# Performance work log

Hardware: AMD Instinct MI355X
Metric: run time of the kernel (lower is better)

## Reference

```python
import jax, jax.numpy as jnp
import numpy as np

N_NODES = 163842
SEQ_LEN = 9
IN_CH = 32
OUT_CH = 64


def setup_inputs() -> dict:
    key = jax.random.key(0)
    k1, k2, k3 = jax.random.split(key, 3)
    x = jax.random.normal(k1, (N_NODES, IN_CH), dtype=jnp.float32)
    indices = jax.random.randint(k2, (N_NODES, SEQ_LEN), 0, N_NODES, dtype=jnp.int64)
    # xavier_uniform for Linear(IN_CH*SEQ_LEN, OUT_CH)
    fan_in = IN_CH * SEQ_LEN
    limit = float(np.sqrt(6.0 / (fan_in + OUT_CH)))
    W = jax.random.uniform(k3, (OUT_CH, fan_in), dtype=jnp.float32, minval=-limit, maxval=limit)
    b = jnp.zeros((OUT_CH,), dtype=jnp.float32)
    return {"x": x, "indices": indices, "W": W, "b": b}


def reference(x, indices, W, b):
    # gather spiral neighbor features: [n_nodes, seq_len, in_ch]
    gathered = x[indices]
    # flatten to [n_nodes, seq_len*in_ch] and apply Linear (y = g @ W^T + b)
    g = gathered.reshape(indices.shape[0], -1)
    return jnp.einsum("nf,of->no", g, W) + b
```

## Files before the change

### kernel.cpp

```cpp
#include <hip/hip_runtime.h>
#include <hip/hip_bf16.h>


constexpr int NN   = 163842;
constexpr int SEQ  = 9;
constexpr int INC  = 32;
constexpr int OUTC = 64;
constexpr int FAN  = SEQ * INC;

using s8    = __attribute__((ext_vector_type(8))) short;
using f32x4 = __attribute__((ext_vector_type(4))) float;

__device__ __forceinline__ unsigned f2bf(float f) {
    union { float f; unsigned u; } c; c.f = f;
    unsigned u = c.u;
    u += 0x7fffu + ((u >> 16) & 1u);
    return (u >> 16) & 0xffffu;
}

__global__ __launch_bounds__(256) void convert_bf16_kernel(
    const float* __restrict__ x, const float* __restrict__ W,
    unsigned short* __restrict__ xb, unsigned short* __restrict__ wb)
{
    const int xq = NN * INC / 4;
    const int wq = OUTC * FAN / 4;
    int i = blockIdx.x * blockDim.x + threadIdx.x;
    if (i < xq) {
        float4 v = reinterpret_cast<const float4*>(x)[i];
        unsigned lo = f2bf(v.x) | (f2bf(v.y) << 16);
        unsigned hi = f2bf(v.z) | (f2bf(v.w) << 16);
        reinterpret_cast<uint2*>(xb)[i] = make_uint2(lo, hi);
    } else if (i < xq + wq) {
        int j = i - xq;
        float4 v = reinterpret_cast<const float4*>(W)[j];
        unsigned lo = f2bf(v.x) | (f2bf(v.y) << 16);
        unsigned hi = f2bf(v.z) | (f2bf(v.w) << 16);
        reinterpret_cast<uint2*>(wb)[j] = make_uint2(lo, hi);
    }
}

__global__ __launch_bounds__(256) void spiral_gemm_kernel(
    const int* __restrict__ idx,
    const unsigned short* __restrict__ xb,
    const unsigned short* __restrict__ wb,
    const float* __restrict__ bias,
    float* __restrict__ out)
{
    const int lane = threadIdx.x & 63;
    const int wid  = threadIdx.x >> 6;
    const int lc   = lane & 15;
    const int lk   = lane >> 4;
    const int kb   = lk * 8;

    const int rowBase = blockIdx.x * 128 + wid * 32;

    f32x4 acc[2][4] = {};

    const int r0 = min(rowBase + lc,      NN - 1);
    const int r1 = min(rowBase + 16 + lc, NN - 1);

    #pragma unroll
    for (int s = 0; s < SEQ; ++s) {
        s8 bfrag[4];
        #pragma unroll
        for (int n = 0; n < 4; ++n) {
            const int o = n * 16 + lc;
            bfrag[n] = *reinterpret_cast<const s8*>(wb + o * FAN + s * 32 + kb);
        }
        const int n0 = idx[r0 * SEQ + s];
        const int n1 = idx[r1 * SEQ + s];
        s8 a0 = *reinterpret_cast<const s8*>(xb + n0 * INC + kb);
        s8 a1 = *reinterpret_cast<const s8*>(xb + n1 * INC + kb);
        #pragma unroll
        for (int n = 0; n < 4; ++n) {
            acc[0][n] = __builtin_amdgcn_mfma_f32_16x16x32_bf16(a0, bfrag[n], acc[0][n], 0, 0, 0);
            acc[1][n] = __builtin_amdgcn_mfma_f32_16x16x32_bf16(a1, bfrag[n], acc[1][n], 0, 0, 0);
        }
    }

    #pragma unroll
    for (int m2 = 0; m2 < 2; ++m2) {
        const int rBase = rowBase + m2 * 16 + lk * 4;
        #pragma unroll
        for (int n = 0; n < 4; ++n) {
            const int o  = n * 16 + lc;
            const float bo = bias[o];
            #pragma unroll
            for (int r = 0; r < 4; ++r) {
                const int row = rBase + r;
                if (row < NN) out[row * OUTC + o] = acc[m2][n][r] + bo;
            }
        }
    }
}

extern "C" void kernel_launch(void* const* d_in, const int* in_sizes, int n_in,
                              void* d_out, int out_size, void* d_ws, size_t ws_size,
                              hipStream_t stream) {
    const float* x    = (const float*)d_in[0];
    const int*   idx  = (const int*)d_in[1];
    const float* W    = (const float*)d_in[2];
    const float* b    = (const float*)d_in[3];
    float*       out  = (float*)d_out;

    unsigned short* xb = (unsigned short*)d_ws;
    unsigned short* wb = xb + (size_t)NN * INC;

    const int totalq = (NN * INC + OUTC * FAN) / 4;
    convert_bf16_kernel<<<(totalq + 255) / 256, 256, 0, stream>>>(x, W, xb, wb);

    const int nblocks = (NN + 127) / 128;
    spiral_gemm_kernel<<<nblocks, 256, 0, stream>>>(idx, xb, wb, b, out);
}
```

Measured before the change: 48.63 us.

## Prefetch all gathered rows upfront and swap MFMA operands for vectorized stores

All nine neighbor indices and their bf16 feature fragments are loaded before any MFMA, so the dependent gather latencies overlap instead of serializing per step. The MFMA operands are swapped (weights as A, features as B), which transposes the accumulator layout so each lane holds four consecutive output channels for one node. That lets the epilogue write float4 stores with a float4 bias load instead of scalar strided stores. The upfront prefetch raises register pressure (18 s8 fragments plus 18 indices), which may lower occupancy.

```diff
diff --git a/kernel.cpp b/kernel.cpp
--- a/kernel.cpp
+++ b/kernel.cpp
@@ -52,43 +52,48 @@
     const int lk   = lane >> 4;
     const int kb   = lk * 8;
 
-    const int rowBase = blockIdx.x * 128 + wid * 32;
+    const int nodeBase = blockIdx.x * 128 + wid * 32;
+
+    const int r0 = min(nodeBase + lc,      NN - 1);
+    const int r1 = min(nodeBase + 16 + lc, NN - 1);
+
+    int n0[SEQ], n1[SEQ];
+    #pragma unroll
+    for (int s = 0; s < SEQ; ++s) {
+        n0[s] = idx[r0 * SEQ + s];
+        n1[s] = idx[r1 * SEQ + s];
+    }
+    s8 xf0[SEQ], xf1[SEQ];
+    #pragma unroll
+    for (int s = 0; s < SEQ; ++s) {
+        xf0[s] = *reinterpret_cast<const s8*>(xb + (size_t)n0[s] * INC + kb);
+        xf1[s] = *reinterpret_cast<const s8*>(xb + (size_t)n1[s] * INC + kb);
+    }
 
     f32x4 acc[2][4] = {};
-
-    const int r0 = min(rowBase + lc,      NN - 1);
-    const int r1 = min(rowBase + 16 + lc, NN - 1);
-
     #pragma unroll
     for (int s = 0; s < SEQ; ++s) {
-        s8 bfrag[4];
         #pragma unroll
-        for (int n = 0; n < 4; ++n) {
-            const int o = n * 16 + lc;
-            bfrag[n] = *reinterpret_cast<const s8*>(wb + o * FAN + s * 32 + kb);
-        }
-        const int n0 = idx[r0 * SEQ + s];
-        const int n1 = idx[r1 * SEQ + s];
-        s8 a0 = *reinterpret_cast<const s8*>(xb + n0 * INC + kb);
-        s8 a1 = *reinterpret_cast<const s8*>(xb + n1 * INC + kb);
-        #pragma unroll
-        for (int n = 0; n < 4; ++n) {
-            acc[0][n] = __builtin_amdgcn_mfma_f32_16x16x32_bf16(a0, bfrag[n], acc[0][n], 0, 0, 0);
-            acc[1][n] = __builtin_amdgcn_mfma_f32_16x16x32_bf16(a1, bfrag[n], acc[1][n], 0, 0, 0);
+        for (int f = 0; f < 4; ++f) {
+            s8 wfrag = *reinterpret_cast<const s8*>(wb + (f * 16 + lc) * FAN + s * 32 + kb);
+            acc[0][f] = __builtin_amdgcn_mfma_f32_16x16x32_bf16(wfrag, xf0[s], acc[0][f], 0, 0, 0);
+            acc[1][f] = __builtin_amdgcn_mfma_f32_16x16x32_bf16(wfrag, xf1[s], acc[1][f], 0, 0, 0);
         }
     }
 
     #pragma unroll
-    for (int m2 = 0; m2 < 2; ++m2) {
-        const int rBase = rowBase + m2 * 16 + lk * 4;
+    for (int f = 0; f < 4; ++f) {
+        const float4 b4 = *reinterpret_cast<const float4*>(bias + f * 16 + lk * 4);
         #pragma unroll
-        for (int n = 0; n < 4; ++n) {
-            const int o  = n * 16 + lc;
-            const float bo = bias[o];
-            #pragma unroll
-            for (int r = 0; r < 4; ++r) {
-                const int row = rBase + r;
-                if (row < NN) out[row * OUTC + o] = acc[m2][n][r] + bo;
+        for (int m = 0; m < 2; ++m) {
+            const int node = nodeBase + m * 16 + lc;
+            if (node < NN) {
+                float4 v;
+                v.x = acc[m][f][0] + b4.x;
+                v.y = acc[m][f][1] + b4.y;
+                v.z = acc[m][f][2] + b4.z;
+                v.w = acc[m][f][3] + b4.w;
+                *reinterpret_cast<float4*>(out + (size_t)node * OUTC + f * 16 + lk * 4) = v;
             }
         }
     }
```

Result: faster. 47.26 us (-2.8%).
